# Kernel tuning notes

Hardware: AMD Instinct MI355X
Metric: run time of the kernel (lower is better)

The kernel has to match this reference:

```python
import jax, jax.numpy as jnp
import numpy as np

N, E, B = 50000, 800000, 2000
EMB, FEAT, L, NTASK = 300, 512, 5, 1
EPS = 1e-5


def setup_inputs() -> dict:
    key = jax.random.key(0)
    ks = jax.random.split(key, 40)
    s = 0.05
    d = {
        'x': jax.random.randint(ks[0], (N, 42), 0, 3),
        'edge_index': jax.random.randint(ks[1], (2, E), 0, N),
        'edge_attr': jax.random.randint(ks[2], (E, 10), 0, 3),
        'batch': jnp.sort(jax.random.randint(ks[3], (N,), 0, B)),
        'x_add': jax.random.normal(ks[4], (B, 200), jnp.float32),
        # atom embeddings
        'atom_e1': jax.random.normal(ks[5], (120, EMB), jnp.float32) * s,
        'atom_e2': jax.random.normal(ks[6], (3, EMB), jnp.float32) * s,
        'atom_w3': jax.random.normal(ks[7], (40, EMB), jnp.float32) * s,
        'atom_b3': jnp.zeros((EMB,), jnp.float32),
        # per-layer GINEConv params (stacked over L layers)
        'edge_e1': jax.random.normal(ks[8], (L, 6, EMB), jnp.float32) * s,
        'edge_e2': jax.random.normal(ks[9], (L, 4, EMB), jnp.float32) * s,
        'edge_w3': jax.random.normal(ks[10], (L, 8, EMB), jnp.float32) * s,
        'edge_b3': jnp.zeros((L, EMB), jnp.float32),
        'mlp_w1': jax.random.normal(ks[11], (L, EMB, 2 * EMB), jnp.float32) * s,
        'mlp_b1': jnp.zeros((L, 2 * EMB), jnp.float32),
        'mlp_w2': jax.random.normal(ks[12], (L, 2 * EMB, EMB), jnp.float32) * s,
        'mlp_b2': jnp.zeros((L, EMB), jnp.float32),
        'bn_g': jnp.ones((L, EMB), jnp.float32),
        'bn_b': jnp.zeros((L, EMB), jnp.float32),
        # feat_lin: emb_dim + 200 -> feat_dim
        'feat_w': jax.random.normal(ks[13], (EMB + 200, FEAT), jnp.float32) * s,
        'feat_b': jnp.zeros((FEAT,), jnp.float32),
        # pred head: 512->256 softplus, 256->256 softplus, 256->1
        'pw1': jax.random.normal(ks[14], (FEAT, FEAT // 2), jnp.float32) * s,
        'pb1': jnp.zeros((FEAT // 2,), jnp.float32),
        'pw2': jax.random.normal(ks[15], (FEAT // 2, FEAT // 2), jnp.float32) * s,
        'pb2': jnp.zeros((FEAT // 2,), jnp.float32),
        'pw3': jax.random.normal(ks[16], (FEAT // 2, NTASK), jnp.float32) * s,
        'pb3': jnp.zeros((NTASK,), jnp.float32),
    }
    return d


def reference(x, edge_index, edge_attr, batch, x_add,
              atom_e1, atom_e2, atom_w3, atom_b3,
              edge_e1, edge_e2, edge_w3, edge_b3,
              mlp_w1, mlp_b1, mlp_w2, mlp_b2, bn_g, bn_b,
              feat_w, feat_b, pw1, pb1, pw2, pb2, pw3, pb3):
    n = x.shape[0]
    nb = x_add.shape[0]

    # node embedding: emb(atom_type) + emb(chirality) + Linear(40 float feats)
    h = (atom_e1[x[:, 0]] + atom_e2[x[:, 1]]
         + x[:, 2:].astype(jnp.float32) @ atom_w3 + atom_b3)

    # add self loops once (same for every layer); self-loop attr: col0=4, rest 0
    loop = jnp.arange(n, dtype=edge_index.dtype)
    src = jnp.concatenate([edge_index[0], loop])
    dst = jnp.concatenate([edge_index[1], loop])
    ea0 = jnp.concatenate([edge_attr[:, 0], jnp.full((n,), 4, edge_attr.dtype)])
    ea1 = jnp.concatenate([edge_attr[:, 1], jnp.zeros((n,), edge_attr.dtype)])
    eaf = jnp.concatenate([edge_attr[:, 2:].astype(jnp.float32),
                           jnp.zeros((n, 8), jnp.float32)], axis=0)

    for l in range(L):
        e_emb = edge_e1[l][ea0] + edge_e2[l][ea1] + eaf @ edge_w3[l] + edge_b3[l]
        msg = h[src] + e_emb                              # [E+N, EMB] gather
        agg = jax.ops.segment_sum(msg, dst, num_segments=n)  # scatter-add
        h = jnp.maximum(agg @ mlp_w1[l] + mlp_b1[l], 0.0) @ mlp_w2[l] + mlp_b2[l]
        # BatchNorm1d (training-mode batch stats, biased var)
        mu = jnp.mean(h, axis=0)
        var = jnp.mean((h - mu) ** 2, axis=0)
        h = (h - mu) * jax.lax.rsqrt(var + EPS) * bn_g[l] + bn_b[l]
        if l != L - 1:
            h = jnp.maximum(h, 0.0)
    h_node = h

    # global mean pool per graph
    sums = jax.ops.segment_sum(h_node, batch, num_segments=nb)
    cnt = jax.ops.segment_sum(jnp.ones((n, 1), h_node.dtype), batch, num_segments=nb)
    pooled = sums / jnp.maximum(cnt, 1.0)

    g = jnp.concatenate([pooled, x_add], axis=1) @ feat_w + feat_b
    g = jax.nn.softplus(g @ pw1 + pb1)
    g = jax.nn.softplus(g @ pw2 + pb2)
    pred = g @ pw3 + pb3
    return h_node, pred
```

## Files before the change

### kernel.cpp

```cpp
#include <hip/hip_runtime.h>
#include <stdint.h>

#define NN 50000
#define EE 800000
#define BG 2000
#define EMB 300
#define HP 320
#define YP 640
#define MPAD 50048
#define MHEAD 2048
#define NLAYER 5

typedef __attribute__((ext_vector_type(8))) _Float16 f16x8;
typedef __attribute__((ext_vector_type(4))) float f32x4;

__device__ __forceinline__ _Float16 f2h(float f) { return (_Float16)f; }

__global__ void k_tconv_all(const float* __restrict__ mw1, const float* __restrict__ mw2,
        const float* __restrict__ fw, const float* __restrict__ pw1, const float* __restrict__ pw2,
        _Float16* __restrict__ w1t, _Float16* __restrict__ w2t, _Float16* __restrict__ fwt,
        _Float16* __restrict__ p1t, _Float16* __restrict__ p2t) {
    int job = blockIdx.x;
    const float* src; _Float16* dst; int K, Ns, Kp, Np;
    if (job < 5)       { src = mw1 + (size_t)job * EMB * 2 * EMB; dst = w1t + (size_t)job * YP * HP; K = EMB; Ns = 2 * EMB; Kp = HP; Np = YP; }
    else if (job < 10) { int l = job - 5; src = mw2 + (size_t)l * 2 * EMB * EMB; dst = w2t + (size_t)l * HP * YP; K = 2 * EMB; Ns = EMB; Kp = YP; Np = HP; }
    else if (job == 10){ src = fw;  dst = fwt; K = 500; Ns = 512; Kp = 512; Np = 512; }
    else if (job == 11){ src = pw1; dst = p1t; K = 512; Ns = 256; Kp = 512; Np = 256; }
    else               { src = pw2; dst = p2t; K = 256; Ns = 256; Kp = 256; Np = 256; }
    int total = Kp * Np;
    for (int idx = blockIdx.y * 256 + threadIdx.x; idx < total; idx += gridDim.y * 256) {
        int n = idx / Kp, k = idx - n * Kp;
        float v = (n < Ns && k < K) ? src[(size_t)k * Ns + n] : 0.f;
        dst[idx] = f2h(v);
    }
}

__global__ void k_padbias_all(const float* __restrict__ mb1, const float* __restrict__ mb2,
                              float* __restrict__ b1p, float* __restrict__ b2p) {
    int idx = blockIdx.x * 256 + threadIdx.x;
    if (idx < NLAYER * YP) {
        int l = idx / YP, c = idx - l * YP;
        b1p[idx] = (c < 2 * EMB) ? mb1[(size_t)l * 2 * EMB + c] : 0.f;
    } else if (idx < NLAYER * YP + NLAYER * HP) {
        int j = idx - NLAYER * YP; int l = j / HP, c = j - l * HP;
        b2p[j] = (c < EMB) ? mb2[(size_t)l * EMB + c] : 0.f;
    }
}

__global__ void k_prep(int* __restrict__ deg, int* __restrict__ cursor,
                       float* __restrict__ psum, float* __restrict__ psq) {
    int i = blockIdx.x * blockDim.x + threadIdx.x;
    if (i < NN) { deg[i] = 0; cursor[i] = 0; }
    if (i < NLAYER * HP) { psum[i] = 0.f; psq[i] = 0.f; }
}

__global__ __launch_bounds__(256) void k_embed(const int* __restrict__ x,
        const float* __restrict__ ae1, const float* __restrict__ ae2,
        const float* __restrict__ aw3, const float* __restrict__ ab3,
        _Float16* __restrict__ h2) {
    int node = blockIdx.x * 4 + (threadIdx.x >> 6);
    int lane = threadIdx.x & 63;
    if (node >= MPAD) return;
    _Float16* outr = h2 + (size_t)node * HP;
    if (node >= NN) {
        #pragma unroll
        for (int j = 0; j < 5; j++) outr[lane + 64 * j] = (_Float16)0.f;
        return;
    }
    const int* xr = x + (size_t)node * 42;
    int x0 = xr[0], x1 = xr[1];
    float acc[5];
    #pragma unroll
    for (int j = 0; j < 5; j++) {
        int c = lane + 64 * j;
        acc[j] = (j < 4 || c < EMB)
               ? (ab3[c] + ae1[(size_t)x0 * EMB + c] + ae2[(size_t)x1 * EMB + c]) : 0.f;
    }
    for (int k = 0; k < 40; k++) {
        float xv = (float)xr[2 + k];
        #pragma unroll
        for (int j = 0; j < 5; j++) {
            int c = lane + 64 * j;
            if (j < 4 || c < EMB) acc[j] = fmaf(xv, aw3[(size_t)k * EMB + c], acc[j]);
        }
    }
    #pragma unroll
    for (int j = 0; j < 5; j++) {
        int c = lane + 64 * j;
        outr[c] = (j < 4 || c < EMB) ? f2h(acc[j]) : (_Float16)0.f;
    }
}

__global__ void k_deg(const int* __restrict__ ei, int* __restrict__ deg) {
    int e = blockIdx.x * blockDim.x + threadIdx.x;
    if (e < EE) atomicAdd(&deg[ei[EE + e]], 1);
}

__global__ __launch_bounds__(1024) void k_scan(const int* __restrict__ deg,
                                               int* __restrict__ rowptr) {
    __shared__ int part[1024];
    int t = threadIdx.x;
    const int chunk = (NN + 1023) / 1024;
    int i0 = t * chunk;
    int i1 = min(i0 + chunk, NN);
    int s = 0;
    for (int i = i0; i < i1; i++) s += deg[i];
    part[t] = s;
    __syncthreads();
    for (int off = 1; off < 1024; off <<= 1) {
        int v = part[t];
        int u = (t >= off) ? part[t - off] : 0;
        __syncthreads();
        part[t] = v + u;
        __syncthreads();
    }
    int run = (t > 0) ? part[t - 1] : 0;
    for (int i = i0; i < i1; i++) { rowptr[i] = run; run += deg[i]; }
    if (t == 1023) rowptr[NN] = part[1023];
}

__global__ void k_fill(const int* __restrict__ ei, const int* __restrict__ ea,
                       const int* __restrict__ rowptr, int* __restrict__ cursor,
                       int* __restrict__ col, unsigned int* __restrict__ eattr) {
    int e = blockIdx.x * blockDim.x + threadIdx.x;
    if (e < EE) {
        int d = ei[EE + e];
        int pos = rowptr[d] + atomicAdd(&cursor[d], 1);
        col[pos] = ei[e];
        unsigned int p = (unsigned int)ea[e * 10 + 0] | ((unsigned int)ea[e * 10 + 1] << 2);
        #pragma unroll
        for (int j = 0; j < 8; j++) p |= (unsigned int)ea[e * 10 + 2 + j] << (4 + 2 * j);
        eattr[pos] = p;
    }
}

__global__ __launch_bounds__(256) void k_stats(const int* __restrict__ rowptr,
        const unsigned int* __restrict__ eattr, int* __restrict__ stat) {
    int node = blockIdx.x * 4 + (threadIdx.x >> 6);
    int lane = threadIdx.x & 63;
    if (node >= NN) return;
    int beg = rowptr[node], end = rowptr[node + 1];
    int c0 = 0, c1 = 0, c2 = 0, d1 = 0, d2 = 0;
    int s[8] = {0, 0, 0, 0, 0, 0, 0, 0};
    for (int e = beg + lane; e < end; e += 64) {
        unsigned int p = eattr[e];
        unsigned int a0 = p & 3u, a1 = (p >> 2) & 3u;
        c0 += (a0 == 0); c1 += (a0 == 1); c2 += (a0 == 2);
        d1 += (a1 == 1); d2 += (a1 == 2);
        #pragma unroll
        for (int j = 0; j < 8; j++) s[j] += (int)((p >> (4 + 2 * j)) & 3u);
    }
    #pragma unroll
    for (int off = 32; off; off >>= 1) {
        c0 += __shfl_down(c0, off); c1 += __shfl_down(c1, off); c2 += __shfl_down(c2, off);
        d1 += __shfl_down(d1, off); d2 += __shfl_down(d2, off);
        #pragma unroll
        for (int j = 0; j < 8; j++) s[j] += __shfl_down(s[j], off);
    }
    if (lane == 0) {
        int dg = end - beg;
        int* st = stat + (size_t)node * 20;
        st[0] = c0; st[1] = c1; st[2] = c2; st[3] = 0; st[4] = 1; st[5] = 0;
        st[6] = dg - d1 - d2 + 1; st[7] = d1; st[8] = d2; st[9] = 0;
        #pragma unroll
        for (int j = 0; j < 8; j++) st[10 + j] = s[j];
        st[18] = dg + 1; st[19] = 0;
    }
}

template<int RELU>
__global__ __launch_bounds__(320) void k_agg(const _Float16* __restrict__ h2,
        const float* __restrict__ psum, const float* __restrict__ psq,
        const float* __restrict__ bng, const float* __restrict__ bnb,
        const int* __restrict__ stat, const int* __restrict__ rowptr,
        const int* __restrict__ col,
        const float* __restrict__ ee1, const float* __restrict__ ee2,
        const float* __restrict__ ew3, const float* __restrict__ eb3,
        _Float16* __restrict__ agg, int layer) {
    int i = blockIdx.x;
    int tid = threadIdx.x;
    if (i >= NN) { agg[(size_t)i * HP + tid] = (_Float16)0.f; return; }
    __shared__ int ss[20];
    if (tid < 20) ss[tid] = stat[(size_t)i * 20 + tid];
    int c = tid;
    bool ch = c < EMB;
    float scl = 0.f, sft = 0.f;
    if (ch) {
        if (RELU) {
            float mu = psum[(size_t)(layer - 1) * HP + c] * (1.f / NN);
            float var = psq[(size_t)(layer - 1) * HP + c] * (1.f / NN) - mu * mu;
            float g = bng[(size_t)(layer - 1) * EMB + c] * rsqrtf(var + 1e-5f);
            scl = g; sft = bnb[(size_t)(layer - 1) * EMB + c] - mu * g;
        } else { scl = 1.f; sft = 0.f; }
    }
    __syncthreads();
    float acc = 0.f;
    if (ch) {
        const float* e1 = ee1 + (size_t)layer * 6 * EMB;
        const float* e2 = ee2 + (size_t)layer * 4 * EMB;
        const float* w3 = ew3 + (size_t)layer * 8 * EMB;
        float v = eb3[(size_t)layer * EMB + c] * (float)ss[18] + e1[4 * EMB + c];
        v = fmaf((float)ss[0], e1[c], v);
        v = fmaf((float)ss[1], e1[EMB + c], v);
        v = fmaf((float)ss[2], e1[2 * EMB + c], v);
        v = fmaf((float)ss[6], e2[c], v);
        v = fmaf((float)ss[7], e2[EMB + c], v);
        v = fmaf((float)ss[8], e2[2 * EMB + c], v);
        #pragma unroll
        for (int k = 0; k < 8; k++) v = fmaf((float)ss[10 + k], w3[k * EMB + c], v);
        acc = v;
    }
    {
        float t = fmaf((float)h2[(size_t)i * HP + c], scl, sft);
        if (RELU) t = fmaxf(t, 0.f);
        acc += t;
    }
    int beg = rowptr[i], end = rowptr[i + 1];
    int e = beg;
    for (; e + 8 <= end; e += 8) {
        int cb[8];
        #pragma unroll
        for (int t = 0; t < 8; t++) cb[t] = col[e + t];
        float vb[8];
        #pragma unroll
        for (int t = 0; t < 8; t++) vb[t] = (float)h2[(size_t)cb[t] * HP + c];
        float tb[8];
        #pragma unroll
        for (int t = 0; t < 8; t++) {
            float tt = fmaf(vb[t], scl, sft);
            if (RELU) tt = fmaxf(tt, 0.f);
            tb[t] = tt;
        }
        acc += ((tb[0] + tb[1]) + (tb[2] + tb[3])) + ((tb[4] + tb[5]) + (tb[6] + tb[7]));
    }
    for (; e < end; ++e) {
        float tt = fmaf((float)h2[(size_t)col[e] * HP + c], scl, sft);
        if (RELU) tt = fmaxf(tt, 0.f);
        acc += tt;
    }
    agg[(size_t)i * HP + tid] = f2h(acc);
}

__global__ __launch_bounds__(256) void k_gemm(const _Float16* __restrict__ A, int lda,
        const _Float16* __restrict__ Wt, int ldw, const float* __restrict__ bias,
        _Float16* __restrict__ C, int ldc, int K, int act, int gridY,
        float* __restrict__ psum, float* __restrict__ psq) {
    __shared__ _Float16 As[2][128 * 32];
    __shared__ _Float16 Bs[2][64 * 32];
    int nwg = gridDim.x;
    int q = nwg >> 3, r = nwg & 7;
    int xcd = blockIdx.x & 7, idx = blockIdx.x >> 3;
    int wg = ((xcd < r) ? xcd * (q + 1) : r * (q + 1) + (xcd - r) * q) + idx;
    int bx = wg / gridY, by = wg - bx * gridY;
    size_t rowBase = (size_t)bx * 128;
    int colBase = by * 64;

    int tid = threadIdx.x, lane = tid & 63, wid = tid >> 6;
    int wr = wid >> 1, wc = wid & 1;
    int srow = tid >> 2, schunk = tid & 3;
    int gchunk = schunk ^ ((srow >> 1) & 3);
    const _Float16* Ab  = A + (rowBase + srow) * (size_t)lda + (gchunk << 3);
    const _Float16* Ab2 = Ab + (size_t)64 * lda;
    const _Float16* Bb  = Wt + ((size_t)colBase + srow) * ldw + (gchunk << 3);
    int ldsbase = wid << 9;

    int lr = lane & 15, lg = lane >> 4;
    int lswz = (lr >> 1) & 3;
    int aoff[4], boff[2];
    #pragma unroll
    for (int m = 0; m < 4; m++) { int rr = wr * 64 + m * 16 + lr; aoff[m] = rr * 32 + ((lg ^ lswz) << 3); }
    #pragma unroll
    for (int n = 0; n < 2; n++) { int rr = wc * 32 + n * 16 + lr; boff[n] = rr * 32 + ((lg ^ lswz) << 3); }

    f32x4 acc[4][2];
    #pragma unroll
    for (int m = 0; m < 4; m++)
        #pragma unroll
        for (int n = 0; n < 2; n++) acc[m][n] = (f32x4){0.f, 0.f, 0.f, 0.f};

    auto stage = [&](int buf, int kt) {
        int o = kt << 5;
        __builtin_amdgcn_global_load_lds(
            (const __attribute__((address_space(1))) void*)(Ab + o),
            (__attribute__((address_space(3))) void*)&As[buf][ldsbase], 16, 0, 0);
        __builtin_amdgcn_global_load_lds(
            (const __attribute__((address_space(1))) void*)(Ab2 + o),
            (__attribute__((address_space(3))) void*)&As[buf][64 * 32 + ldsbase], 16, 0, 0);
        __builtin_amdgcn_global_load_lds(
            (const __attribute__((address_space(1))) void*)(Bb + o),
            (__attribute__((address_space(3))) void*)&Bs[buf][ldsbase], 16, 0, 0);
    };

    int nk = K >> 5;
    stage(0, 0);
    __syncthreads();
    int cur = 0;
    for (int kt = 0; kt < nk; ++kt) {
        if (kt + 1 < nk) stage(cur ^ 1, kt + 1);
        f16x8 af[4], bfr[2];
        #pragma unroll
        for (int m = 0; m < 4; m++) af[m] = *(const f16x8*)&As[cur][aoff[m]];
        #pragma unroll
        for (int n = 0; n < 2; n++) bfr[n] = *(const f16x8*)&Bs[cur][boff[n]];
        #pragma unroll
        for (int m = 0; m < 4; m++)
            #pragma unroll
            for (int n = 0; n < 2; n++)
                acc[m][n] = __builtin_amdgcn_mfma_f32_16x16x32_f16(af[m], bfr[n], acc[m][n], 0, 0, 0);
        __syncthreads();
        cur ^= 1;
    }

    bool dostats = (psum != nullptr);
    float sstat[2] = {0.f, 0.f}, qstat[2] = {0.f, 0.f};
    #pragma unroll
    for (int m = 0; m < 4; m++) {
        #pragma unroll
        for (int n = 0; n < 2; n++) {
            int colg = colBase + wc * 32 + n * 16 + lr;
            float bv = bias[colg];
            #pragma unroll
            for (int rj = 0; rj < 4; rj++) {
                size_t rowg = rowBase + wr * 64 + m * 16 + lg * 4 + rj;
                float v = acc[m][n][rj] + bv;
                if (act == 1) v = fmaxf(v, 0.f);
                else if (act == 2) v = (v > 0.f) ? v + log1pf(expf(-v)) : log1pf(expf(v));
                C[rowg * ldc + colg] = f2h(v);
                if (dostats && rowg < NN) { sstat[n] += v; qstat[n] += v * v; }
            }
        }
    }
    if (dostats) {
        #pragma unroll
        for (int n = 0; n < 2; n++) {
            float s_ = sstat[n], q_ = qstat[n];
            s_ += __shfl_xor(s_, 16); q_ += __shfl_xor(q_, 16);
            s_ += __shfl_xor(s_, 32); q_ += __shfl_xor(q_, 32);
            if (lane < 16) {
                int colg = colBase + wc * 32 + n * 16 + lr;
                atomicAdd(&psum[colg], s_);
                atomicAdd(&psq[colg], q_);
            }
        }
    }
}

__global__ __launch_bounds__(256) void k_bn_apply(const _Float16* __restrict__ h2,
        const float* __restrict__ psum, const float* __restrict__ psq,
        const float* __restrict__ bng, const float* __restrict__ bnb,
        float* __restrict__ out) {
    int node = blockIdx.x * 4 + (threadIdx.x >> 6);
    int lane = threadIdx.x & 63;
    if (node >= NN) return;
    const float* ps = psum + (size_t)(NLAYER - 1) * HP;
    const float* pq = psq  + (size_t)(NLAYER - 1) * HP;
    const float* g_ = bng + (size_t)(NLAYER - 1) * EMB;
    const float* b_ = bnb + (size_t)(NLAYER - 1) * EMB;
    #pragma unroll
    for (int j = 0; j < 5; j++) {
        int c = lane + 64 * j;
        if (j < 4 || c < EMB) {
            float mu = ps[c] * (1.f / NN);
            float var = pq[c] * (1.f / NN) - mu * mu;
            float g = g_[c] * rsqrtf(var + 1e-5f);
            out[(size_t)node * EMB + c] =
                fmaf((float)h2[(size_t)node * HP + c], g, b_[c] - mu * g);
        }
    }
}

__global__ __launch_bounds__(512) void k_pool(const float* __restrict__ hn,
        const int* __restrict__ batch, const float* __restrict__ x_add,
        _Float16* __restrict__ hin) {
    int b = blockIdx.x, c = threadIdx.x;
    if (b >= BG) { hin[(size_t)b * 512 + c] = (_Float16)0.f; return; }
    __shared__ int sb[2];
    if (c < 2) {
        int target = b + c;
        int lo = 0, hi = NN;
        while (lo < hi) { int mid = (lo + hi) >> 1; if (batch[mid] < target) lo = mid + 1; else hi = mid; }
        sb[c] = lo;
    }
    __syncthreads();
    float v = 0.f;
    if (c < EMB) {
        int s = sb[0], e = sb[1];
        float a = 0.f;
        for (int i = s; i < e; i++) a += hn[(size_t)i * EMB + c];
        v = a / (float)max(e - s, 1);
    } else if (c < EMB + 200) {
        v = x_add[(size_t)b * 200 + (c - EMB)];
    }
    hin[(size_t)b * 512 + c] = f2h(v);
}

__global__ __launch_bounds__(64) void k_pred(const _Float16* __restrict__ g3,
        const float* __restrict__ pw3, const float* __restrict__ pb3, float* __restrict__ out) {
    int row = blockIdx.x;
    int lane = threadIdx.x;
    float s = 0.f;
    #pragma unroll
    for (int t = 0; t < 4; t++) {
        int k = lane * 4 + t;
        s += (float)g3[(size_t)row * 256 + k] * pw3[k];
    }
    #pragma unroll
    for (int off = 32; off; off >>= 1) s += __shfl_down(s, off);
    if (lane == 0) out[row] = s + pb3[0];
}

extern "C" void kernel_launch(void* const* d_in, const int* in_sizes, int n_in,
                              void* d_out, int out_size, void* d_ws, size_t ws_size,
                              hipStream_t stream) {
    const int*   x     = (const int*)d_in[0];
    const int*   ei    = (const int*)d_in[1];
    const int*   ea    = (const int*)d_in[2];
    const int*   batch = (const int*)d_in[3];
    const float* x_add = (const float*)d_in[4];
    const float* ae1   = (const float*)d_in[5];
    const float* ae2   = (const float*)d_in[6];
    const float* aw3   = (const float*)d_in[7];
    const float* ab3   = (const float*)d_in[8];
    const float* ee1   = (const float*)d_in[9];
    const float* ee2   = (const float*)d_in[10];
    const float* ew3   = (const float*)d_in[11];
    const float* eb3   = (const float*)d_in[12];
    const float* mw1   = (const float*)d_in[13];
    const float* mb1   = (const float*)d_in[14];
    const float* mw2   = (const float*)d_in[15];
    const float* mb2   = (const float*)d_in[16];
    const float* bng   = (const float*)d_in[17];
    const float* bnb   = (const float*)d_in[18];
    const float* fw    = (const float*)d_in[19];
    const float* fb    = (const float*)d_in[20];
    const float* pw1   = (const float*)d_in[21];
    const float* pb1   = (const float*)d_in[22];
    const float* pw2   = (const float*)d_in[23];
    const float* pb2   = (const float*)d_in[24];
    const float* pw3   = (const float*)d_in[25];
    const float* pb3   = (const float*)d_in[26];
    (void)in_sizes; (void)n_in; (void)out_size; (void)ws_size;
    float* out = (float*)d_out;

    char* p = (char*)d_ws;
    auto take = [&](size_t bytes) -> char* {
        char* r = p; p += (bytes + 255) & ~(size_t)255; return r;
    };
    _Float16*  h2   = (_Float16*)take((size_t)MPAD * HP * 2);
    _Float16*  agg  = (_Float16*)take((size_t)MPAD * HP * 2);
    _Float16*  y1   = (_Float16*)take((size_t)MPAD * YP * 2);
    _Float16*  w1t  = (_Float16*)take((size_t)NLAYER * YP * HP * 2);
    _Float16*  w2t  = (_Float16*)take((size_t)NLAYER * HP * YP * 2);
    _Float16*  fwt  = (_Float16*)take((size_t)512 * 512 * 2);
    _Float16*  p1t  = (_Float16*)take((size_t)256 * 512 * 2);
    _Float16*  p2t  = (_Float16*)take((size_t)256 * 256 * 2);
    float* b1p    = (float*)take((size_t)NLAYER * YP * 4);
    float* b2p    = (float*)take((size_t)NLAYER * HP * 4);
    int* deg      = (int*)take((size_t)NN * 4);
    int* cursor   = (int*)take((size_t)NN * 4);
    int* rowptr   = (int*)take((size_t)(NN + 1) * 4);
    int* col      = (int*)take((size_t)EE * 4);
    unsigned int* eattr = (unsigned int*)take((size_t)EE * 4);
    int* stat     = (int*)take((size_t)NN * 20 * 4);
    float* psum   = (float*)take((size_t)NLAYER * HP * 4);
    float* psq    = (float*)take((size_t)NLAYER * HP * 4);
    char* hb = (char*)y1;
    _Float16* hin = (_Float16*)hb;  hb += (size_t)MHEAD * 512 * 2;
    _Float16* g1  = (_Float16*)hb;  hb += (size_t)MHEAD * 512 * 2;
    _Float16* g2  = (_Float16*)hb;  hb += (size_t)MHEAD * 256 * 2;
    _Float16* g3  = (_Float16*)hb;

    k_prep<<<(NN + 255) / 256, 256, 0, stream>>>(deg, cursor, psum, psq);
    k_tconv_all<<<dim3(13, 1024), 256, 0, stream>>>(mw1, mw2, fw, pw1, pw2, w1t, w2t, fwt, p1t, p2t);
    k_padbias_all<<<19, 256, 0, stream>>>(mb1, mb2, b1p, b2p);
    k_embed<<<(MPAD + 3) / 4, 256, 0, stream>>>(x, ae1, ae2, aw3, ab3, h2);
    k_deg<<<(EE + 255) / 256, 256, 0, stream>>>(ei, deg);
    k_scan<<<1, 1024, 0, stream>>>(deg, rowptr);
    k_fill<<<(EE + 255) / 256, 256, 0, stream>>>(ei, ea, rowptr, cursor, col, eattr);
    k_stats<<<(NN + 3) / 4, 256, 0, stream>>>(rowptr, eattr, stat);

    const int MT = MPAD / 128;
    for (int l = 0; l < NLAYER; l++) {
        if (l == 0)
            k_agg<0><<<MPAD, 320, 0, stream>>>(h2, psum, psq, bng, bnb,
                stat, rowptr, col, ee1, ee2, ew3, eb3, agg, l);
        else
            k_agg<1><<<MPAD, 320, 0, stream>>>(h2, psum, psq, bng, bnb,
                stat, rowptr, col, ee1, ee2, ew3, eb3, agg, l);
        k_gemm<<<MT * (YP / 64), 256, 0, stream>>>(
            agg, HP, w1t + (size_t)l * YP * HP, HP, b1p + (size_t)l * YP,
            y1, YP, HP, 1, YP / 64, nullptr, nullptr);
        k_gemm<<<MT * (HP / 64), 256, 0, stream>>>(
            y1, YP, w2t + (size_t)l * HP * YP, YP, b2p + (size_t)l * HP,
            h2, HP, YP, 0, HP / 64, psum + (size_t)l * HP, psq + (size_t)l * HP);
    }
    k_bn_apply<<<(NN + 3) / 4, 256, 0, stream>>>(h2, psum, psq, bng, bnb, out);

    k_pool<<<MHEAD, 512, 0, stream>>>(out, batch, x_add, hin);
    k_gemm<<<(MHEAD / 128) * (512 / 64), 256, 0, stream>>>(hin, 512, fwt, 512, fb, g1, 512, 512, 0, 512 / 64, nullptr, nullptr);
    k_gemm<<<(MHEAD / 128) * (256 / 64), 256, 0, stream>>>(g1, 512, p1t, 512, pb1, g2, 256, 512, 2, 256 / 64, nullptr, nullptr);
    k_gemm<<<(MHEAD / 128) * (256 / 64), 256, 0, stream>>>(g2, 256, p2t, 256, pb2, g3, 256, 256, 2, 256 / 64, nullptr, nullptr);
    k_pred<<<BG, 64, 0, stream>>>(g3, pw3, pb3, out + (size_t)NN * EMB);
}
```

Measured before the change: 1.773 ms.

## Merge setup kernels, enlarge GEMM row tile to 256, fuse final BN into pooling

Several small setup kernels (weight transpose, bias padding, buffer zeroing, atom embedding) are combined into one launch to cut launch overhead. The GEMM tile grows from 128 to 256 rows per block with 8x2 MFMA accumulators per wave, which improves reuse of the B tile but doubles LDS and register use and halves the number of blocks. The last-layer BatchNorm apply is folded into the pooling kernel, which now writes the normalized output as it sums. This removes one full pass over the node features, at the cost of serializing those writes per graph inside each pooling block.

Measured after the change: 1.941 ms. 1.09x slower.

```diff
diff --git a/kernel.cpp b/kernel.cpp
--- a/kernel.cpp
+++ b/kernel.cpp
@@ -7,87 +7,90 @@
 #define EMB 300
 #define HP 320
 #define YP 640
-#define MPAD 50048
+#define MPAD 50176
 #define MHEAD 2048
 #define NLAYER 5
 
+#define TCB 3328
+#define EMBB (MPAD/4)
+#define MISCB 196
+
 typedef __attribute__((ext_vector_type(8))) _Float16 f16x8;
 typedef __attribute__((ext_vector_type(4))) float f32x4;
 
 __device__ __forceinline__ _Float16 f2h(float f) { return (_Float16)f; }
 
-__global__ void k_tconv_all(const float* __restrict__ mw1, const float* __restrict__ mw2,
+__global__ __launch_bounds__(256) void k_setup(
+        const float* __restrict__ mw1, const float* __restrict__ mw2,
         const float* __restrict__ fw, const float* __restrict__ pw1, const float* __restrict__ pw2,
+        const float* __restrict__ mb1, const float* __restrict__ mb2,
+        const int* __restrict__ x, const float* __restrict__ ae1, const float* __restrict__ ae2,
+        const float* __restrict__ aw3, const float* __restrict__ ab3,
         _Float16* __restrict__ w1t, _Float16* __restrict__ w2t, _Float16* __restrict__ fwt,
-        _Float16* __restrict__ p1t, _Float16* __restrict__ p2t) {
-    int job = blockIdx.x;
-    const float* src; _Float16* dst; int K, Ns, Kp, Np;
-    if (job < 5)       { src = mw1 + (size_t)job * EMB * 2 * EMB; dst = w1t + (size_t)job * YP * HP; K = EMB; Ns = 2 * EMB; Kp = HP; Np = YP; }
-    else if (job < 10) { int l = job - 5; src = mw2 + (size_t)l * 2 * EMB * EMB; dst = w2t + (size_t)l * HP * YP; K = 2 * EMB; Ns = EMB; Kp = YP; Np = HP; }
-    else if (job == 10){ src = fw;  dst = fwt; K = 500; Ns = 512; Kp = 512; Np = 512; }
-    else if (job == 11){ src = pw1; dst = p1t; K = 512; Ns = 256; Kp = 512; Np = 256; }
-    else               { src = pw2; dst = p2t; K = 256; Ns = 256; Kp = 256; Np = 256; }
-    int total = Kp * Np;
-    for (int idx = blockIdx.y * 256 + threadIdx.x; idx < total; idx += gridDim.y * 256) {
-        int n = idx / Kp, k = idx - n * Kp;
-        float v = (n < Ns && k < K) ? src[(size_t)k * Ns + n] : 0.f;
-        dst[idx] = f2h(v);
-    }
-}
-
-__global__ void k_padbias_all(const float* __restrict__ mb1, const float* __restrict__ mb2,
-                              float* __restrict__ b1p, float* __restrict__ b2p) {
-    int idx = blockIdx.x * 256 + threadIdx.x;
-    if (idx < NLAYER * YP) {
-        int l = idx / YP, c = idx - l * YP;
-        b1p[idx] = (c < 2 * EMB) ? mb1[(size_t)l * 2 * EMB + c] : 0.f;
-    } else if (idx < NLAYER * YP + NLAYER * HP) {
-        int j = idx - NLAYER * YP; int l = j / HP, c = j - l * HP;
-        b2p[j] = (c < EMB) ? mb2[(size_t)l * EMB + c] : 0.f;
-    }
-}
-
-__global__ void k_prep(int* __restrict__ deg, int* __restrict__ cursor,
-                       float* __restrict__ psum, float* __restrict__ psq) {
-    int i = blockIdx.x * blockDim.x + threadIdx.x;
+        _Float16* __restrict__ p1t, _Float16* __restrict__ p2t,
+        float* __restrict__ b1p, float* __restrict__ b2p,
+        int* __restrict__ deg, int* __restrict__ cursor,
+        float* __restrict__ psum, float* __restrict__ psq,
+        _Float16* __restrict__ h2) {
+    int b = blockIdx.x, tid = threadIdx.x;
+    if (b < TCB) {
+        int job = b >> 8, sub = b & 255;
+        const float* src; _Float16* dst; int K, Ns, Kp, Np;
+        if (job < 5)       { src = mw1 + (size_t)job * EMB * 2 * EMB; dst = w1t + (size_t)job * YP * HP; K = EMB; Ns = 2 * EMB; Kp = HP; Np = YP; }
+        else if (job < 10) { int l = job - 5; src = mw2 + (size_t)l * 2 * EMB * EMB; dst = w2t + (size_t)l * HP * YP; K = 2 * EMB; Ns = EMB; Kp = YP; Np = HP; }
+        else if (job == 10){ src = fw;  dst = fwt; K = 500; Ns = 512; Kp = 512; Np = 512; }
+        else if (job == 11){ src = pw1; dst = p1t; K = 512; Ns = 256; Kp = 512; Np = 256; }
+        else               { src = pw2; dst = p2t; K = 256; Ns = 256; Kp = 256; Np = 256; }
+        int total = Kp * Np;
+        for (int idx = sub * 256 + tid; idx < total; idx += 256 * 256) {
+            int n = idx / Kp, k = idx - n * Kp;
+            float v = (n < Ns && k < K) ? src[(size_t)k * Ns + n] : 0.f;
+            dst[idx] = f2h(v);
+        }
+        return;
+    }
+    if (b < TCB + EMBB) {
+        int node = (b - TCB) * 4 + (tid >> 6);
+        int lane = tid & 63;
+        _Float16* outr = h2 + (size_t)node * HP;
+        if (node >= NN) {
+            #pragma unroll
+            for (int j = 0; j < 5; j++) outr[lane + 64 * j] = (_Float16)0.f;
+            return;
+        }
+        const int* xr = x + (size_t)node * 42;
+        int x0 = xr[0], x1 = xr[1];
+        float acc[5];
+        #pragma unroll
+        for (int j = 0; j < 5; j++) {
+            int c = lane + 64 * j;
+            acc[j] = (j < 4 || c < EMB)
+                   ? (ab3[c] + ae1[(size_t)x0 * EMB + c] + ae2[(size_t)x1 * EMB + c]) : 0.f;
+        }
+        for (int k = 0; k < 40; k++) {
+            float xv = (float)xr[2 + k];
+            #pragma unroll
+            for (int j = 0; j < 5; j++) {
+                int c = lane + 64 * j;
+                if (j < 4 || c < EMB) acc[j] = fmaf(xv, aw3[(size_t)k * EMB + c], acc[j]);
+            }
+        }
+        #pragma unroll
+        for (int j = 0; j < 5; j++) {
+            int c = lane + 64 * j;
+            outr[c] = (j < 4 || c < EMB) ? f2h(acc[j]) : (_Float16)0.f;
+        }
+        return;
+    }
+    int i = (b - TCB - EMBB) * 256 + tid;
     if (i < NN) { deg[i] = 0; cursor[i] = 0; }
     if (i < NLAYER * HP) { psum[i] = 0.f; psq[i] = 0.f; }
-}
-
-__global__ __launch_bounds__(256) void k_embed(const int* __restrict__ x,
-        const float* __restrict__ ae1, const float* __restrict__ ae2,
-        const float* __restrict__ aw3, const float* __restrict__ ab3,
-        _Float16* __restrict__ h2) {
-    int node = blockIdx.x * 4 + (threadIdx.x >> 6);
-    int lane = threadIdx.x & 63;
-    if (node >= MPAD) return;
-    _Float16* outr = h2 + (size_t)node * HP;
-    if (node >= NN) {
-        #pragma unroll
-        for (int j = 0; j < 5; j++) outr[lane + 64 * j] = (_Float16)0.f;
-        return;
-    }
-    const int* xr = x + (size_t)node * 42;
-    int x0 = xr[0], x1 = xr[1];
-    float acc[5];
-    #pragma unroll
-    for (int j = 0; j < 5; j++) {
-        int c = lane + 64 * j;
-        acc[j] = (j < 4 || c < EMB)
-               ? (ab3[c] + ae1[(size_t)x0 * EMB + c] + ae2[(size_t)x1 * EMB + c]) : 0.f;
-    }
-    for (int k = 0; k < 40; k++) {
-        float xv = (float)xr[2 + k];
-        #pragma unroll
-        for (int j = 0; j < 5; j++) {
-            int c = lane + 64 * j;
-            if (j < 4 || c < EMB) acc[j] = fmaf(xv, aw3[(size_t)k * EMB + c], acc[j]);
-        }
-    }
-    #pragma unroll
-    for (int j = 0; j < 5; j++) {
-        int c = lane + 64 * j;
-        outr[c] = (j < 4 || c < EMB) ? f2h(acc[j]) : (_Float16)0.f;
+    if (i < NLAYER * YP) {
+        int l = i / YP, c = i - l * YP;
+        b1p[i] = (c < 2 * EMB) ? mb1[(size_t)l * 2 * EMB + c] : 0.f;
+    } else if (i < NLAYER * YP + NLAYER * HP) {
+        int j = i - NLAYER * YP; int l = j / HP, c = j - l * HP;
+        b2p[j] = (c < EMB) ? mb2[(size_t)l * EMB + c] : 0.f;
     }
 }
 
@@ -245,47 +248,46 @@
         const _Float16* __restrict__ Wt, int ldw, const float* __restrict__ bias,
         _Float16* __restrict__ C, int ldc, int K, int act, int gridY,
         float* __restrict__ psum, float* __restrict__ psq) {
-    __shared__ _Float16 As[2][128 * 32];
+    __shared__ _Float16 As[2][256 * 32];
     __shared__ _Float16 Bs[2][64 * 32];
     int nwg = gridDim.x;
     int q = nwg >> 3, r = nwg & 7;
     int xcd = blockIdx.x & 7, idx = blockIdx.x >> 3;
     int wg = ((xcd < r) ? xcd * (q + 1) : r * (q + 1) + (xcd - r) * q) + idx;
     int bx = wg / gridY, by = wg - bx * gridY;
-    size_t rowBase = (size_t)bx * 128;
+    size_t rowBase = (size_t)bx * 256;
     int colBase = by * 64;
 
     int tid = threadIdx.x, lane = tid & 63, wid = tid >> 6;
     int wr = wid >> 1, wc = wid & 1;
     int srow = tid >> 2, schunk = tid & 3;
     int gchunk = schunk ^ ((srow >> 1) & 3);
-    const _Float16* Ab  = A + (rowBase + srow) * (size_t)lda + (gchunk << 3);
-    const _Float16* Ab2 = Ab + (size_t)64 * lda;
-    const _Float16* Bb  = Wt + ((size_t)colBase + srow) * ldw + (gchunk << 3);
+    const _Float16* Ab = A + (rowBase + srow) * (size_t)lda + (gchunk << 3);
+    const _Float16* Bb = Wt + ((size_t)colBase + srow) * ldw + (gchunk << 3);
     int ldsbase = wid << 9;
 
     int lr = lane & 15, lg = lane >> 4;
     int lswz = (lr >> 1) & 3;
-    int aoff[4], boff[2];
-    #pragma unroll
-    for (int m = 0; m < 4; m++) { int rr = wr * 64 + m * 16 + lr; aoff[m] = rr * 32 + ((lg ^ lswz) << 3); }
+    int aoff[8], boff[2];
+    #pragma unroll
+    for (int m = 0; m < 8; m++) { int rr = wr * 128 + m * 16 + lr; aoff[m] = rr * 32 + ((lg ^ lswz) << 3); }
     #pragma unroll
     for (int n = 0; n < 2; n++) { int rr = wc * 32 + n * 16 + lr; boff[n] = rr * 32 + ((lg ^ lswz) << 3); }
 
-    f32x4 acc[4][2];
-    #pragma unroll
-    for (int m = 0; m < 4; m++)
+    f32x4 acc[8][2];
+    #pragma unroll
+    for (int m = 0; m < 8; m++)
         #pragma unroll
         for (int n = 0; n < 2; n++) acc[m][n] = (f32x4){0.f, 0.f, 0.f, 0.f};
 
     auto stage = [&](int buf, int kt) {
         int o = kt << 5;
-        __builtin_amdgcn_global_load_lds(
-            (const __attribute__((address_space(1))) void*)(Ab + o),
-            (__attribute__((address_space(3))) void*)&As[buf][ldsbase], 16, 0, 0);
-        __builtin_amdgcn_global_load_lds(
-            (const __attribute__((address_space(1))) void*)(Ab2 + o),
-            (__attribute__((address_space(3))) void*)&As[buf][64 * 32 + ldsbase], 16, 0, 0);
+        #pragma unroll
+        for (int i2 = 0; i2 < 4; i2++) {
+            __builtin_amdgcn_global_load_lds(
+                (const __attribute__((address_space(1))) void*)(Ab + (size_t)i2 * 64 * lda + o),
+                (__attribute__((address_space(3))) void*)&As[buf][i2 * 64 * 32 + ldsbase], 16, 0, 0);
+        }
         __builtin_amdgcn_global_load_lds(
             (const __attribute__((address_space(1))) void*)(Bb + o),
             (__attribute__((address_space(3))) void*)&Bs[buf][ldsbase], 16, 0, 0);
@@ -297,13 +299,13 @@
     int cur = 0;
     for (int kt = 0; kt < nk; ++kt) {
         if (kt + 1 < nk) stage(cur ^ 1, kt + 1);
-        f16x8 af[4], bfr[2];
-        #pragma unroll
-        for (int m = 0; m < 4; m++) af[m] = *(const f16x8*)&As[cur][aoff[m]];
+        f16x8 af[8], bfr[2];
+        #pragma unroll
+        for (int m = 0; m < 8; m++) af[m] = *(const f16x8*)&As[cur][aoff[m]];
         #pragma unroll
         for (int n = 0; n < 2; n++) bfr[n] = *(const f16x8*)&Bs[cur][boff[n]];
         #pragma unroll
-        for (int m = 0; m < 4; m++)
+        for (int m = 0; m < 8; m++)
             #pragma unroll
             for (int n = 0; n < 2; n++)
                 acc[m][n] = __builtin_amdgcn_mfma_f32_16x16x32_f16(af[m], bfr[n], acc[m][n], 0, 0, 0);
@@ -312,66 +314,39 @@
     }
 
     bool dostats = (psum != nullptr);
-    float sstat[2] = {0.f, 0.f}, qstat[2] = {0.f, 0.f};
-    #pragma unroll
-    for (int m = 0; m < 4; m++) {
-        #pragma unroll
-        for (int n = 0; n < 2; n++) {
-            int colg = colBase + wc * 32 + n * 16 + lr;
-            float bv = bias[colg];
+    #pragma unroll
+    for (int n = 0; n < 2; n++) {
+        int colg = colBase + wc * 32 + n * 16 + lr;
+        float bv = bias[colg];
+        float sstat = 0.f, qstat = 0.f;
+        #pragma unroll
+        for (int m = 0; m < 8; m++) {
             #pragma unroll
             for (int rj = 0; rj < 4; rj++) {
-                size_t rowg = rowBase + wr * 64 + m * 16 + lg * 4 + rj;
+                size_t rowg = rowBase + wr * 128 + m * 16 + lg * 4 + rj;
                 float v = acc[m][n][rj] + bv;
                 if (act == 1) v = fmaxf(v, 0.f);
                 else if (act == 2) v = (v > 0.f) ? v + log1pf(expf(-v)) : log1pf(expf(v));
                 C[rowg * ldc + colg] = f2h(v);
-                if (dostats && rowg < NN) { sstat[n] += v; qstat[n] += v * v; }
+                if (dostats && rowg < NN) { sstat += v; qstat += v * v; }
             }
         }
-    }
-    if (dostats) {
-        #pragma unroll
-        for (int n = 0; n < 2; n++) {
-            float s_ = sstat[n], q_ = qstat[n];
-            s_ += __shfl_xor(s_, 16); q_ += __shfl_xor(q_, 16);
-            s_ += __shfl_xor(s_, 32); q_ += __shfl_xor(q_, 32);
+        if (dostats) {
+            sstat += __shfl_xor(sstat, 16); qstat += __shfl_xor(qstat, 16);
+            sstat += __shfl_xor(sstat, 32); qstat += __shfl_xor(qstat, 32);
             if (lane < 16) {
-                int colg = colBase + wc * 32 + n * 16 + lr;
-                atomicAdd(&psum[colg], s_);
-                atomicAdd(&psq[colg], q_);
+                atomicAdd(&psum[colg], sstat);
+                atomicAdd(&psq[colg], qstat);
             }
         }
     }
 }
 
-__global__ __launch_bounds__(256) void k_bn_apply(const _Float16* __restrict__ h2,
+__global__ __launch_bounds__(512) void k_pool(const _Float16* __restrict__ h2,
         const float* __restrict__ psum, const float* __restrict__ psq,
         const float* __restrict__ bng, const float* __restrict__ bnb,
-        float* __restrict__ out) {
-    int node = blockIdx.x * 4 + (threadIdx.x >> 6);
-    int lane = threadIdx.x & 63;
-    if (node >= NN) return;
-    const float* ps = psum + (size_t)(NLAYER - 1) * HP;
-    const float* pq = psq  + (size_t)(NLAYER - 1) * HP;
-    const float* g_ = bng + (size_t)(NLAYER - 1) * EMB;
-    const float* b_ = bnb + (size_t)(NLAYER - 1) * EMB;
-    #pragma unroll
-    for (int j = 0; j < 5; j++) {
-        int c = lane + 64 * j;
-        if (j < 4 || c < EMB) {
-            float mu = ps[c] * (1.f / NN);
-            float var = pq[c] * (1.f / NN) - mu * mu;
-            float g = g_[c] * rsqrtf(var + 1e-5f);
-            out[(size_t)node * EMB + c] =
-                fmaf((float)h2[(size_t)node * HP + c], g, b_[c] - mu * g);
-        }
-    }
-}
-
-__global__ __launch_bounds__(512) void k_pool(const float* __restrict__ hn,
         const int* __restrict__ batch, const float* __restrict__ x_add,
-        _Float16* __restrict__ hin) {
+        float* __restrict__ out, _Float16* __restrict__ hin) {
     int b = blockIdx.x, c = threadIdx.x;
     if (b >= BG) { hin[(size_t)b * 512 + c] = (_Float16)0.f; return; }
     __shared__ int sb[2];
@@ -384,9 +359,17 @@
     __syncthreads();
     float v = 0.f;
     if (c < EMB) {
+        float mu = psum[(size_t)(NLAYER - 1) * HP + c] * (1.f / NN);
+        float var = psq[(size_t)(NLAYER - 1) * HP + c] * (1.f / NN) - mu * mu;
+        float g = bng[(size_t)(NLAYER - 1) * EMB + c] * rsqrtf(var + 1e-5f);
+        float off = bnb[(size_t)(NLAYER - 1) * EMB + c] - mu * g;
         int s = sb[0], e = sb[1];
         float a = 0.f;
-        for (int i = s; i < e; i++) a += hn[(size_t)i * EMB + c];
+        for (int i = s; i < e; i++) {
+            float hv = fmaf((float)h2[(size_t)i * HP + c], g, off);
+            out[(size_t)i * EMB + c] = hv;
+            a += hv;
+        }
         v = a / (float)max(e - s, 1);
     } else if (c < EMB + 200) {
         v = x_add[(size_t)b * 200 + (c - EMB)];
@@ -470,16 +453,15 @@
     _Float16* g2  = (_Float16*)hb;  hb += (size_t)MHEAD * 256 * 2;
     _Float16* g3  = (_Float16*)hb;
 
-    k_prep<<<(NN + 255) / 256, 256, 0, stream>>>(deg, cursor, psum, psq);
-    k_tconv_all<<<dim3(13, 1024), 256, 0, stream>>>(mw1, mw2, fw, pw1, pw2, w1t, w2t, fwt, p1t, p2t);
-    k_padbias_all<<<19, 256, 0, stream>>>(mb1, mb2, b1p, b2p);
-    k_embed<<<(MPAD + 3) / 4, 256, 0, stream>>>(x, ae1, ae2, aw3, ab3, h2);
+    k_setup<<<TCB + EMBB + MISCB, 256, 0, stream>>>(
+        mw1, mw2, fw, pw1, pw2, mb1, mb2, x, ae1, ae2, aw3, ab3,
+        w1t, w2t, fwt, p1t, p2t, b1p, b2p, deg, cursor, psum, psq, h2);
     k_deg<<<(EE + 255) / 256, 256, 0, stream>>>(ei, deg);
     k_scan<<<1, 1024, 0, stream>>>(deg, rowptr);
     k_fill<<<(EE + 255) / 256, 256, 0, stream>>>(ei, ea, rowptr, cursor, col, eattr);
     k_stats<<<(NN + 3) / 4, 256, 0, stream>>>(rowptr, eattr, stat);
 
-    const int MT = MPAD / 128;
+    const int MT = MPAD / 256;
     for (int l = 0; l < NLAYER; l++) {
         if (l == 0)
             k_agg<0><<<MPAD, 320, 0, stream>>>(h2, psum, psq, bng, bnb,
@@ -494,11 +476,10 @@
             y1, YP, w2t + (size_t)l * HP * YP, YP, b2p + (size_t)l * HP,
             h2, HP, YP, 0, HP / 64, psum + (size_t)l * HP, psq + (size_t)l * HP);
     }
-    k_bn_apply<<<(NN + 3) / 4, 256, 0, stream>>>(h2, psum, psq, bng, bnb, out);
-
-    k_pool<<<MHEAD, 512, 0, stream>>>(out, batch, x_add, hin);
-    k_gemm<<<(MHEAD / 128) * (512 / 64), 256, 0, stream>>>(hin, 512, fwt, 512, fb, g1, 512, 512, 0, 512 / 64, nullptr, nullptr);
-    k_gemm<<<(MHEAD / 128) * (256 / 64), 256, 0, stream>>>(g1, 512, p1t, 512, pb1, g2, 256, 512, 2, 256 / 64, nullptr, nullptr);
-    k_gemm<<<(MHEAD / 128) * (256 / 64), 256, 0, stream>>>(g2, 256, p2t, 256, pb2, g3, 256, 256, 2, 256 / 64, nullptr, nullptr);
+
+    k_pool<<<MHEAD, 512, 0, stream>>>(h2, psum, psq, bng, bnb, batch, x_add, out, hin);
+    k_gemm<<<(MHEAD / 256) * (512 / 64), 256, 0, stream>>>(hin, 512, fwt, 512, fb, g1, 512, 512, 0, 512 / 64, nullptr, nullptr);
+    k_gemm<<<(MHEAD / 256) * (256 / 64), 256, 0, stream>>>(g1, 512, p1t, 512, pb1, g2, 256, 512, 2, 256 / 64, nullptr, nullptr);
+    k_gemm<<<(MHEAD / 256) * (256 / 64), 256, 0, stream>>>(g2, 256, p2t, 256, pb2, g3, 256, 256, 2, 256 / 64, nullptr, nullptr);
     k_pred<<<BG, 64, 0, stream>>>(g3, pw3, pb3, out + (size_t)NN * EMB);
 }
```
